# Performance work log

Measured on AMD Instinct MI355X. Metric: run time of the kernel, lower is better.

The kernel has to match this reference:

```python
import jax, jax.numpy as jnp
import numpy as np

N_NODES = 10000
N_EDGES = 160000
N_FEATS = 9       # OGB atom features
VOCAB = 128       # >= max atom feature cardinality (119)
D = 128           # d_input == d_atom_emb
H = 4             # n_heads
C = 128           # out_channels per head (== d_input)
L = 3             # n_layers
N_CLASSES = 10
NEG_SLOPE = 0.2   # PyG GATConv default


def setup_inputs() -> dict:
    key = jax.random.key(0)
    ks = jax.random.split(key, 10)
    nodes_features = jax.random.randint(ks[0], (N_NODES, N_FEATS), 0, 119, dtype=jnp.int64)
    edges_connectivity = jax.random.randint(ks[1], (2, N_EDGES), 0, N_NODES, dtype=jnp.int64)
    s = 1.0 / np.sqrt(D)
    emb_tables = jax.random.normal(ks[2], (N_FEATS, VOCAB, D), dtype=jnp.float32) * s
    W = jax.random.normal(ks[3], (L, D, H * C), dtype=jnp.float32) * s
    att_src = jax.random.normal(ks[4], (L, H, C), dtype=jnp.float32) * s
    att_dst = jax.random.normal(ks[5], (L, H, C), dtype=jnp.float32) * s
    bias = jnp.zeros((L, C), dtype=jnp.float32)
    Wc = jax.random.normal(ks[6], (D, N_CLASSES), dtype=jnp.float32) * s
    bc = jnp.zeros((N_CLASSES,), dtype=jnp.float32)
    return {"nodes_features": nodes_features, "edges_connectivity": edges_connectivity,
            "emb_tables": emb_tables, "W": W, "att_src": att_src, "att_dst": att_dst,
            "bias": bias, "Wc": Wc, "bc": bc}


def _gat_layer(x, src, dst, W_l, a_s, a_d, b_l):
    # x: [N, D] -> h: [N, H, C]
    h = (x @ W_l).reshape(-1, H, C)
    alpha_src = jnp.einsum('nhc,hc->nh', h, a_s)  # [N, H]
    alpha_dst = jnp.einsum('nhc,hc->nh', h, a_d)  # [N, H]
    e = alpha_src[src] + alpha_dst[dst]           # [E, H]
    e = jnp.where(e >= 0, e, NEG_SLOPE * e)       # LeakyReLU(0.2)
    # segment softmax over edges grouped by destination node
    m = jax.ops.segment_max(e, dst, num_segments=N_NODES)  # [N, H]
    ex = jnp.exp(e - m[dst])
    s = jax.ops.segment_sum(ex, dst, num_segments=N_NODES)  # [N, H]
    alpha = ex / (s[dst] + 1e-16)                 # [E, H]
    msg = h[src] * alpha[..., None]               # [E, H, C]
    out = jax.ops.segment_sum(msg, dst, num_segments=N_NODES)  # [N, H, C]
    return out.mean(axis=1) + b_l                 # concat=False: mean over heads


def reference(nodes_features, edges_connectivity, emb_tables, W, att_src, att_dst, bias, Wc, bc):
    # AtomEncoder: sum per-feature embeddings -> [N, D]
    x = emb_tables[jnp.arange(N_FEATS), nodes_features].sum(axis=1)
    src, dst = edges_connectivity[0], edges_connectivity[1]
    for i in range(L):
        # dropout treated as identity (eval-mode reference)
        x = _gat_layer(x, src, dst, W[i], att_src[i], att_dst[i], bias[i])
        if i < L - 1:
            x = jax.nn.gelu(x)
    pooled = x.mean(axis=0)                       # graph mean-pool over nodes -> [D]
    return pooled @ Wc + bc                       # [n_classes]
```

## Files before the change

### kernel.cpp

```cpp
#include <hip/hip_runtime.h>
#include <hip/hip_bf16.h>
#include <math.h>

#define NN 10000
#define NE 160000
#define NF 9
#define VOCAB 128
#define D 128
#define NH 4
#define C 128
#define HC 512
#define NCLS 10
#define NL 3

#define NEG_BIG (-1e30f)

typedef __attribute__((ext_vector_type(8))) short bf16x8;
typedef __attribute__((ext_vector_type(4))) float f32x4;

__device__ __forceinline__ unsigned short f2bf(float f) {
    unsigned u = __float_as_uint(f);
    unsigned r = ((u >> 16) & 1u) + 0x7FFFu;
    return (unsigned short)((u + r) >> 16);
}
__device__ __forceinline__ float bf2f(unsigned short h) {
    return __uint_as_float(((unsigned)h) << 16);
}

__global__ __launch_bounds__(256)
void hist(const int* __restrict__ dst, int* __restrict__ deg) {
    int e = blockIdx.x * 256 + threadIdx.x;
    if (e < NE) atomicAdd(&deg[dst[e]], 1);
}

#define SCAN_T 1024
#define SCAN_PER ((NN + SCAN_T - 1) / SCAN_T)
__global__ __launch_bounds__(SCAN_T)
void scan_deg(const int* __restrict__ deg, int* __restrict__ rowstart,
              int* __restrict__ cursor) {
    __shared__ int part[SCAN_T];
    int t = threadIdx.x;
    int base = t * SCAN_PER;
    int vals[SCAN_PER];
    int loc = 0;
#pragma unroll
    for (int i = 0; i < SCAN_PER; ++i) {
        int idx = base + i;
        int v = (idx < NN) ? deg[idx] : 0;
        vals[i] = v;
        loc += v;
    }
    part[t] = loc;
    __syncthreads();
    for (int off = 1; off < SCAN_T; off <<= 1) {
        int y = (t >= off) ? part[t - off] : 0;
        __syncthreads();
        part[t] += y;
        __syncthreads();
    }
    int run = part[t] - loc;
#pragma unroll
    for (int i = 0; i < SCAN_PER; ++i) {
        int idx = base + i;
        if (idx < NN) { rowstart[idx] = run; cursor[idx] = run; }
        run += vals[i];
    }
}

__global__ __launch_bounds__(256)
void scatter(const int* __restrict__ src, const int* __restrict__ dst,
             int* __restrict__ cursor, int* __restrict__ csr_src) {
    int e = blockIdx.x * 256 + threadIdx.x;
    if (e < NE) {
        int p = atomicAdd(&cursor[dst[e]], 1);
        csr_src[p] = src[e];
    }
}

__global__ __launch_bounds__(512)
void prep_all(const float* __restrict__ W, const float* __restrict__ as_,
              const float* __restrict__ ad_, const float* __restrict__ Wc,
              const float* __restrict__ biasA, const float* __restrict__ bc,
              float* __restrict__ wsrc, float* __restrict__ wdst,
              unsigned short* __restrict__ Bth, unsigned short* __restrict__ Btl,
              float* __restrict__ M, float* __restrict__ b10,
              float* __restrict__ p512) {
    int b = blockIdx.x;
    if (b < 24) {
        int k = threadIdx.x;
        if (k >= 128) return;
        int l = b >> 3;
        int r = b & 7;
        int h = r >> 1;
        int side = r & 1;
        const float* av = (side ? ad_ : as_) + (size_t)(l * NH + h) * C;
        const float* wrow = W + (size_t)l * D * HC + (size_t)k * HC + h * C;
        float acc = 0.f;
#pragma unroll 4
        for (int c = 0; c < C; ++c) acc += wrow[c] * av[c];
        float* o = (side ? wdst : wsrc) + (size_t)(l * NH + h) * D + k;
        *o = acc;
    } else if (b < 280) {
        int bb = b - 24;
        int l = bb >> 7;
        int c = bb & 127;
        int j = threadIdx.x;
        float v = W[(size_t)l * D * HC + (size_t)(j >> 2) * HC + (j & 3) * C + c];
        unsigned short h = f2bf(v);
        unsigned short lo = f2bf(v - bf2f(h));
        size_t o = (size_t)(l * 128 + c) * HC + j;
        Bth[o] = h;
        Btl[o] = lo;
    } else {
        int k = b - 280;
        int j = threadIdx.x;
        const float* W3 = W + (size_t)2 * D * HC;
        const float* bias3 = biasA + (size_t)2 * D;
        const float* wrow = W3 + (size_t)(j >> 2) * HC + (j & 3) * C;
        float acc = 0.f;
#pragma unroll 4
        for (int c = 0; c < C; ++c) acc += wrow[c] * Wc[c * NCLS + k];
        M[(size_t)k * HC + j] = acc;
        if (k == 0) p512[j] = 0.f;
        if (j == 0) {
            float bsum = bc[k];
            for (int c = 0; c < C; ++c) bsum += bias3[c] * Wc[c * NCLS + k];
            b10[k] = bsum;
        }
    }
}

__global__ __launch_bounds__(128)
void atom_encoder_alpha(const int* __restrict__ feats, const float* __restrict__ emb,
                        const float* __restrict__ wsrc0, const float* __restrict__ wdst0,
                        float* __restrict__ x, float* __restrict__ asrc,
                        float* __restrict__ adst) {
    int n = blockIdx.x;
    int t = threadIdx.x;
    __shared__ int f[NF];
    __shared__ float part[2][8];
    if (t < NF) f[t] = feats[n * NF + t];
    __syncthreads();
    float acc = 0.f;
#pragma unroll
    for (int i = 0; i < NF; ++i)
        acc += emb[(i * VOCAB + f[i]) * D + t];
    x[n * D + t] = acc;

    float dots[8];
#pragma unroll
    for (int h = 0; h < NH; ++h) {
        dots[h]     = acc * wsrc0[h * D + t];
        dots[4 + h] = acc * wdst0[h * D + t];
    }
#pragma unroll
    for (int off = 32; off; off >>= 1)
#pragma unroll
        for (int k = 0; k < 8; ++k) dots[k] += __shfl_down(dots[k], off);
    if ((t & 63) == 0) {
        int w = t >> 6;
#pragma unroll
        for (int k = 0; k < 8; ++k) part[w][k] = dots[k];
    }
    __syncthreads();
    if (t < 8) {
        float v = part[0][t] + part[1][t];
        if (t < 4) asrc[n * NH + t] = v;
        else       adst[n * NH + (t - 4)] = v;
    }
}

__global__ __launch_bounds__(256)
void alphas2(const float* __restrict__ X, const float* __restrict__ wsrc,
             const float* __restrict__ wdst, float* __restrict__ asrc,
             float* __restrict__ adst) {
    int n = blockIdx.x * 4 + (threadIdx.x >> 6);
    int lane = threadIdx.x & 63;
    float x0 = X[n * D + lane], x1 = X[n * D + lane + 64];
#pragma unroll
    for (int h = 0; h < NH; ++h) {
        float s = x0 * wsrc[h * D + lane] + x1 * wsrc[h * D + lane + 64];
        float d = x0 * wdst[h * D + lane] + x1 * wdst[h * D + lane + 64];
#pragma unroll
        for (int off = 32; off; off >>= 1) {
            s += __shfl_down(s, off);
            d += __shfl_down(d, off);
        }
        if (lane == 0) { asrc[n * NH + h] = s; adst[n * NH + h] = d; }
    }
}

__global__ __launch_bounds__(128)
void gat_agg(const int* __restrict__ csr_src, const int* __restrict__ rowstart,
             const int* __restrict__ degA, const float* __restrict__ asr,
             const float* __restrict__ adr, const float* __restrict__ X,
             unsigned* __restrict__ aggh, unsigned* __restrict__ aggl) {
    int n = blockIdx.x;
    int t = threadIdx.x;
    int deg = degA[n];
    int start = rowstart[n];

    __shared__ float smax[NH];
    __shared__ float sinv[NH];
    __shared__ float lal[128][NH];
    __shared__ int lsrc[128];

    int h = t >> 5, i = t & 31;
    float ad_h = adr[n * NH + h];
    float mx = NEG_BIG;
    for (int j = i; j < deg; j += 32) {
        int s = csr_src[start + j];
        float v = asr[s * NH + h] + ad_h;
        v = v >= 0.f ? v : 0.2f * v;
        mx = fmaxf(mx, v);
    }
#pragma unroll
    for (int off = 16; off; off >>= 1) mx = fmaxf(mx, __shfl_xor(mx, off));
    if (i == 0) smax[h] = mx;
    __syncthreads();
    float m = smax[h];
    float ss = 0.f;
    for (int j = i; j < deg; j += 32) {
        int s = csr_src[start + j];
        float v = asr[s * NH + h] + ad_h;
        v = v >= 0.f ? v : 0.2f * v;
        ss += __expf(v - m);
    }
#pragma unroll
    for (int off = 16; off; off >>= 1) ss += __shfl_xor(ss, off);
    if (i == 0) sinv[h] = 0.25f / (ss + 1e-16f);
    __syncthreads();

    float fm0 = smax[0], fm1 = smax[1], fm2 = smax[2], fm3 = smax[3];
    float fi0 = sinv[0], fi1 = sinv[1], fi2 = sinv[2], fi3 = sinv[3];
    float a0 = adr[n * NH + 0], a1 = adr[n * NH + 1];
    float a2 = adr[n * NH + 2], a3 = adr[n * NH + 3];
    float acc0 = 0.f, acc1 = 0.f, acc2 = 0.f, acc3 = 0.f;

    for (int cb = 0; cb < deg; cb += 128) {
        int cl = deg - cb; if (cl > 128) cl = 128;
        if (t < cl) {
            int sn = csr_src[start + cb + t];
            float4 av = *(const float4*)(asr + sn * NH);
            float v0 = av.x + a0; v0 = v0 >= 0.f ? v0 : 0.2f * v0;
            float v1 = av.y + a1; v1 = v1 >= 0.f ? v1 : 0.2f * v1;
            float v2 = av.z + a2; v2 = v2 >= 0.f ? v2 : 0.2f * v2;
            float v3 = av.w + a3; v3 = v3 >= 0.f ? v3 : 0.2f * v3;
            lal[t][0] = __expf(v0 - fm0) * fi0;
            lal[t][1] = __expf(v1 - fm1) * fi1;
            lal[t][2] = __expf(v2 - fm2) * fi2;
            lal[t][3] = __expf(v3 - fm3) * fi3;
            lsrc[t] = sn;
        }
        __syncthreads();
#pragma unroll 4
        for (int j = 0; j < cl; ++j) {
            float xv = X[(size_t)lsrc[j] * D + t];
            float4 w = *(const float4*)lal[j];
            acc0 += w.x * xv;
            acc1 += w.y * xv;
            acc2 += w.z * xv;
            acc3 += w.w * xv;
        }
        __syncthreads();
    }

    unsigned short h0 = f2bf(acc0), h1 = f2bf(acc1), h2 = f2bf(acc2), h3 = f2bf(acc3);
    unsigned short l0 = f2bf(acc0 - bf2f(h0)), l1 = f2bf(acc1 - bf2f(h1));
    unsigned short l2 = f2bf(acc2 - bf2f(h2)), l3 = f2bf(acc3 - bf2f(h3));
    size_t base = ((size_t)n * HC + t * 4) >> 1;
    uint2 uh = make_uint2((unsigned)h0 | ((unsigned)h1 << 16),
                          (unsigned)h2 | ((unsigned)h3 << 16));
    uint2 ul = make_uint2((unsigned)l0 | ((unsigned)l1 << 16),
                          (unsigned)l2 | ((unsigned)l3 << 16));
    *(uint2*)(aggh + base) = uh;
    *(uint2*)(aggl + base) = ul;
}

__global__ __launch_bounds__(64)
void gemm_mfma(const unsigned short* __restrict__ Ah, const unsigned short* __restrict__ Al,
               const unsigned short* __restrict__ Bth, const unsigned short* __restrict__ Btl,
               const float* __restrict__ bias, float* __restrict__ Out, int do_gelu) {
    int lane = threadIdx.x;
    int m0 = blockIdx.x * 16;
    int n0 = blockIdx.y * 64;
    int r = lane & 15;
    int g = lane >> 4;

    const bf16x8* ah = (const bf16x8*)(Ah + (size_t)(m0 + r) * HC + g * 8);
    const bf16x8* al = (const bf16x8*)(Al + (size_t)(m0 + r) * HC + g * 8);
    const bf16x8* bh0 = (const bf16x8*)(Bth + (size_t)(n0 + 0 * 16 + r) * HC + g * 8);
    const bf16x8* bh1 = (const bf16x8*)(Bth + (size_t)(n0 + 1 * 16 + r) * HC + g * 8);
    const bf16x8* bh2 = (const bf16x8*)(Bth + (size_t)(n0 + 2 * 16 + r) * HC + g * 8);
    const bf16x8* bh3 = (const bf16x8*)(Bth + (size_t)(n0 + 3 * 16 + r) * HC + g * 8);
    const bf16x8* bl0 = (const bf16x8*)(Btl + (size_t)(n0 + 0 * 16 + r) * HC + g * 8);
    const bf16x8* bl1 = (const bf16x8*)(Btl + (size_t)(n0 + 1 * 16 + r) * HC + g * 8);
    const bf16x8* bl2 = (const bf16x8*)(Btl + (size_t)(n0 + 2 * 16 + r) * HC + g * 8);
    const bf16x8* bl3 = (const bf16x8*)(Btl + (size_t)(n0 + 3 * 16 + r) * HC + g * 8);

    f32x4 acc[4];
#pragma unroll
    for (int q = 0; q < 4; ++q) acc[q] = (f32x4){0.f, 0.f, 0.f, 0.f};

#pragma unroll 2
    for (int ks = 0; ks < HC / 32; ++ks) {
        bf16x8 a_h = ah[ks * 4];
        bf16x8 a_l = al[ks * 4];
        bf16x8 b;
        b = bh0[ks * 4];
        acc[0] = __builtin_amdgcn_mfma_f32_16x16x32_bf16(a_h, b, acc[0], 0, 0, 0);
        acc[0] = __builtin_amdgcn_mfma_f32_16x16x32_bf16(a_l, b, acc[0], 0, 0, 0);
        b = bl0[ks * 4];
        acc[0] = __builtin_amdgcn_mfma_f32_16x16x32_bf16(a_h, b, acc[0], 0, 0, 0);
        b = bh1[ks * 4];
        acc[1] = __builtin_amdgcn_mfma_f32_16x16x32_bf16(a_h, b, acc[1], 0, 0, 0);
        acc[1] = __builtin_amdgcn_mfma_f32_16x16x32_bf16(a_l, b, acc[1], 0, 0, 0);
        b = bl1[ks * 4];
        acc[1] = __builtin_amdgcn_mfma_f32_16x16x32_bf16(a_h, b, acc[1], 0, 0, 0);
        b = bh2[ks * 4];
        acc[2] = __builtin_amdgcn_mfma_f32_16x16x32_bf16(a_h, b, acc[2], 0, 0, 0);
        acc[2] = __builtin_amdgcn_mfma_f32_16x16x32_bf16(a_l, b, acc[2], 0, 0, 0);
        b = bl2[ks * 4];
        acc[2] = __builtin_amdgcn_mfma_f32_16x16x32_bf16(a_h, b, acc[2], 0, 0, 0);
        b = bh3[ks * 4];
        acc[3] = __builtin_amdgcn_mfma_f32_16x16x32_bf16(a_h, b, acc[3], 0, 0, 0);
        acc[3] = __builtin_amdgcn_mfma_f32_16x16x32_bf16(a_l, b, acc[3], 0, 0, 0);
        b = bl3[ks * 4];
        acc[3] = __builtin_amdgcn_mfma_f32_16x16x32_bf16(a_h, b, acc[3], 0, 0, 0);
    }

#pragma unroll
    for (int q = 0; q < 4; ++q) {
#pragma unroll
        for (int i = 0; i < 4; ++i) {
            int row = m0 + g * 4 + i;
            int col = n0 + q * 16 + r;
            float v = acc[q][i] + bias[col];
            if (do_gelu) {
                float u = 0.7978845608028654f * (v + 0.044715f * v * v * v);
                v = 0.5f * v * (1.f + tanhf(u));
            }
            Out[(size_t)row * D + col] = v;
        }
    }
}

__global__ __launch_bounds__(512)
void pool512(const unsigned short* __restrict__ Ah, const unsigned short* __restrict__ Al,
             float* __restrict__ p) {
    int t = threadIdx.x;
    int chunk = (NN + gridDim.x - 1) / gridDim.x;
    int n0 = blockIdx.x * chunk;
    int n1 = n0 + chunk; if (n1 > NN) n1 = NN;
    float acc = 0.f;
    for (int n = n0; n < n1; ++n)
        acc += bf2f(Ah[(size_t)n * HC + t]) + bf2f(Al[(size_t)n * HC + t]);
    atomicAdd(p + t, acc);
}

__global__ __launch_bounds__(640)
void final10(const float* __restrict__ p512, const float* __restrict__ M,
             const float* __restrict__ b10, float* __restrict__ out) {
    int k = threadIdx.x >> 6;
    int lane = threadIdx.x & 63;
    float acc = 0.f;
#pragma unroll
    for (int i = 0; i < HC / 64; ++i) {
        int j = lane + i * 64;
        acc += p512[j] * M[(size_t)k * HC + j];
    }
#pragma unroll
    for (int off = 32; off; off >>= 1) acc += __shfl_down(acc, off);
    if (lane == 0) out[k] = b10[k] + acc * (1.0f / NN);
}

extern "C" void kernel_launch(void* const* d_in, const int* in_sizes, int n_in,
                              void* d_out, int out_size, void* d_ws, size_t ws_size,
                              hipStream_t stream) {
    const int*   feats = (const int*)d_in[0];
    const int*   edges = (const int*)d_in[1];
    const float* emb   = (const float*)d_in[2];
    const float* W     = (const float*)d_in[3];
    const float* asrcW = (const float*)d_in[4];
    const float* adstW = (const float*)d_in[5];
    const float* bias  = (const float*)d_in[6];
    const float* Wc    = (const float*)d_in[7];
    const float* bc    = (const float*)d_in[8];
    float* out = (float*)d_out;

    const int* srcp = edges;
    const int* dstp = edges + NE;

    char* ws = (char*)d_ws;
    size_t off = 0;
    unsigned short* aggh = (unsigned short*)(ws + off); off += (size_t)NN * HC * 2;
    unsigned short* aggl = (unsigned short*)(ws + off); off += (size_t)NN * HC * 2;
    float* xb0    = (float*)(ws + off); off += (size_t)NN * D * 4;
    float* xb1    = (float*)(ws + off); off += (size_t)NN * D * 4;
    float* asrc   = (float*)(ws + off); off += (size_t)NN * NH * 4;
    float* adst   = (float*)(ws + off); off += (size_t)NN * NH * 4;
    int*   deg    = (int*)(ws + off);   off += (size_t)NN * 4;
    int*   rowst  = (int*)(ws + off);   off += (size_t)NN * 4;
    int*   cursor = (int*)(ws + off);   off += (size_t)NN * 4;
    int*   csrsrc = (int*)(ws + off);   off += (size_t)NE * 4;
    float* wsrcb  = (float*)(ws + off); off += (size_t)NL * NH * D * 4;
    float* wdstb  = (float*)(ws + off); off += (size_t)NL * NH * D * 4;
    unsigned short* Bth = (unsigned short*)(ws + off); off += (size_t)2 * 128 * HC * 2;
    unsigned short* Btl = (unsigned short*)(ws + off); off += (size_t)2 * 128 * HC * 2;
    float* Mhead  = (float*)(ws + off); off += (size_t)NCLS * HC * 4;
    float* b10    = (float*)(ws + off); off += NCLS * 4;
    float* p512   = (float*)(ws + off); off += HC * 4;

    hipMemsetAsync(deg, 0, (size_t)NN * 4, stream);
    hist<<<(NE + 255) / 256, 256, 0, stream>>>(dstp, deg);
    scan_deg<<<1, SCAN_T, 0, stream>>>(deg, rowst, cursor);
    scatter<<<(NE + 255) / 256, 256, 0, stream>>>(srcp, dstp, cursor, csrsrc);
    prep_all<<<290, 512, 0, stream>>>(W, asrcW, adstW, Wc, bias, bc,
                                      wsrcb, wdstb, Bth, Btl, Mhead, b10, p512);

    atom_encoder_alpha<<<NN, 128, 0, stream>>>(feats, emb, wsrcb, wdstb,
                                               xb0, asrc, adst);

    float* xin = xb0;
    float* xout = xb1;
    for (int l = 0; l < 2; ++l) {
        if (l > 0)
            alphas2<<<NN / 4, 256, 0, stream>>>(xin, wsrcb + (size_t)l * NH * D,
                                                wdstb + (size_t)l * NH * D, asrc, adst);
        gat_agg<<<NN, 128, 0, stream>>>(csrsrc, rowst, deg, asrc, adst, xin,
                                        (unsigned*)aggh, (unsigned*)aggl);
        gemm_mfma<<<dim3(NN / 16, 2), 64, 0, stream>>>(
            aggh, aggl, Bth + (size_t)l * 128 * HC, Btl + (size_t)l * 128 * HC,
            bias + (size_t)l * D, xout, 1);
        float* tmp = xin; xin = xout; xout = tmp;
    }

    alphas2<<<NN / 4, 256, 0, stream>>>(xin, wsrcb + (size_t)2 * NH * D,
                                        wdstb + (size_t)2 * NH * D, asrc, adst);
    gat_agg<<<NN, 128, 0, stream>>>(csrsrc, rowst, deg, asrc, adst, xin,
                                    (unsigned*)aggh, (unsigned*)aggl);
    pool512<<<100, 512, 0, stream>>>(aggh, aggl, p512);
    final10<<<1, 640, 0, stream>>>(p512, Mhead, b10, out);
}
```

Before: 296.7 us.

## Fuse whole GAT pipeline into one cooperative persistent kernel with grid syncs

Replaces the sequence of about fifteen kernel launches (histogram, scan, scatter, prep, encoder, per-layer alphas/aggregation/GEMM, pooling, head) with a single cooperative kernel of 512 blocks that separates phases with grid-wide syncs. Aggregation now handles two nodes per 256-thread block in a grid-stride loop, and the GEMM maps four 64-thread tiles per block. The goal is to remove launch overhead and inter-kernel gaps, at the cost of grid-sync latency, lower occupancy per phase, and the added barriers in aggregation when two nodes with different degrees share a block. The old multi-kernel path is kept as a fallback if the cooperative launch fails.

After: 1.159 ms. +290.5%, slower.

```diff
diff --git a/kernel.cpp b/kernel.cpp
--- a/kernel.cpp
+++ b/kernel.cpp
@@ -1,6 +1,9 @@
 #include <hip/hip_runtime.h>
 #include <hip/hip_bf16.h>
+#include <hip/hip_cooperative_groups.h>
 #include <math.h>
+
+namespace cg = cooperative_groups;
 
 #define NN 10000
 #define NE 160000
@@ -14,6 +17,8 @@
 #define NL 3
 
 #define NEG_BIG (-1e30f)
+#define MB 512
+#define NCHUNK 20
 
 typedef __attribute__((ext_vector_type(8))) short bf16x8;
 typedef __attribute__((ext_vector_type(4))) float f32x4;
@@ -27,263 +32,125 @@
     return __uint_as_float(((unsigned)h) << 16);
 }
 
-__global__ __launch_bounds__(256)
-void hist(const int* __restrict__ dst, int* __restrict__ deg) {
-    int e = blockIdx.x * 256 + threadIdx.x;
-    if (e < NE) atomicAdd(&deg[dst[e]], 1);
-}
-
-#define SCAN_T 1024
-#define SCAN_PER ((NN + SCAN_T - 1) / SCAN_T)
-__global__ __launch_bounds__(SCAN_T)
-void scan_deg(const int* __restrict__ deg, int* __restrict__ rowstart,
-              int* __restrict__ cursor) {
-    __shared__ int part[SCAN_T];
-    int t = threadIdx.x;
-    int base = t * SCAN_PER;
-    int vals[SCAN_PER];
-    int loc = 0;
-#pragma unroll
-    for (int i = 0; i < SCAN_PER; ++i) {
-        int idx = base + i;
-        int v = (idx < NN) ? deg[idx] : 0;
-        vals[i] = v;
-        loc += v;
-    }
-    part[t] = loc;
-    __syncthreads();
-    for (int off = 1; off < SCAN_T; off <<= 1) {
-        int y = (t >= off) ? part[t - off] : 0;
+
+struct MegaParams {
+    const int* feats; const int* srcp; const int* dstp;
+    const float* emb; const float* W; const float* asrcW; const float* adstW;
+    const float* bias; const float* Wc; const float* bc;
+    float* out;
+    unsigned short *aggh, *aggl;
+    float *xb0, *xb1, *asrc, *adst;
+    int *deg, *rowst, *cursor, *csrsrc, *blocksum, *blockoff;
+    float *wsrcb, *wdstb;
+    unsigned short *Bth, *Btl;
+    float *Mhead, *b10, *p512;
+};
+
+__device__ __forceinline__ void run_agg(
+    const int* __restrict__ csr, const int* __restrict__ rowstA,
+    const int* __restrict__ degA, const float* __restrict__ asr,
+    const float* __restrict__ adr, const float* __restrict__ X,
+    unsigned* __restrict__ aggh, unsigned* __restrict__ aggl,
+    int tid, int bid,
+    float* smax, float* sinv, float* lal, int* lsrc, int* sdeg) {
+    int sub = tid >> 7, tt = tid & 127;
+    for (int base = 0; base < NN; base += MB * 2) {
+        int n = base + bid * 2 + sub;
+        bool valid = n < NN;
+        int deg = valid ? degA[n] : 0;
+        int start = valid ? rowstA[n] : 0;
+        int h = tt >> 5, i = tt & 31;
+        float ad_h = valid ? adr[n * NH + h] : 0.f;
+        float mx = NEG_BIG;
+        for (int j = i; j < deg; j += 32) {
+            int s = csr[start + j];
+            float v = asr[s * NH + h] + ad_h;
+            v = v >= 0.f ? v : 0.2f * v;
+            mx = fmaxf(mx, v);
+        }
+#pragma unroll
+        for (int off = 16; off; off >>= 1) mx = fmaxf(mx, __shfl_xor(mx, off));
+        if (i == 0) smax[sub * NH + h] = mx;
         __syncthreads();
-        part[t] += y;
+        float m = smax[sub * NH + h];
+        float ss = 0.f;
+        for (int j = i; j < deg; j += 32) {
+            int s = csr[start + j];
+            float v = asr[s * NH + h] + ad_h;
+            v = v >= 0.f ? v : 0.2f * v;
+            ss += __expf(v - m);
+        }
+#pragma unroll
+        for (int off = 16; off; off >>= 1) ss += __shfl_xor(ss, off);
+        if (i == 0) sinv[sub * NH + h] = 0.25f / (ss + 1e-16f);
+        if (tt == 0) sdeg[sub] = deg;
         __syncthreads();
-    }
-    int run = part[t] - loc;
-#pragma unroll
-    for (int i = 0; i < SCAN_PER; ++i) {
-        int idx = base + i;
-        if (idx < NN) { rowstart[idx] = run; cursor[idx] = run; }
-        run += vals[i];
-    }
-}
-
-__global__ __launch_bounds__(256)
-void scatter(const int* __restrict__ src, const int* __restrict__ dst,
-             int* __restrict__ cursor, int* __restrict__ csr_src) {
-    int e = blockIdx.x * 256 + threadIdx.x;
-    if (e < NE) {
-        int p = atomicAdd(&cursor[dst[e]], 1);
-        csr_src[p] = src[e];
-    }
-}
-
-__global__ __launch_bounds__(512)
-void prep_all(const float* __restrict__ W, const float* __restrict__ as_,
-              const float* __restrict__ ad_, const float* __restrict__ Wc,
-              const float* __restrict__ biasA, const float* __restrict__ bc,
-              float* __restrict__ wsrc, float* __restrict__ wdst,
-              unsigned short* __restrict__ Bth, unsigned short* __restrict__ Btl,
-              float* __restrict__ M, float* __restrict__ b10,
-              float* __restrict__ p512) {
-    int b = blockIdx.x;
-    if (b < 24) {
-        int k = threadIdx.x;
-        if (k >= 128) return;
-        int l = b >> 3;
-        int r = b & 7;
-        int h = r >> 1;
-        int side = r & 1;
-        const float* av = (side ? ad_ : as_) + (size_t)(l * NH + h) * C;
-        const float* wrow = W + (size_t)l * D * HC + (size_t)k * HC + h * C;
-        float acc = 0.f;
+
+        float fm0 = smax[sub * NH + 0], fm1 = smax[sub * NH + 1];
+        float fm2 = smax[sub * NH + 2], fm3 = smax[sub * NH + 3];
+        float fi0 = sinv[sub * NH + 0], fi1 = sinv[sub * NH + 1];
+        float fi2 = sinv[sub * NH + 2], fi3 = sinv[sub * NH + 3];
+        float a0 = 0.f, a1 = 0.f, a2 = 0.f, a3 = 0.f;
+        if (valid) {
+            float4 av = *(const float4*)(adr + n * NH);
+            a0 = av.x; a1 = av.y; a2 = av.z; a3 = av.w;
+        }
+        int dmax = sdeg[0] > sdeg[1] ? sdeg[0] : sdeg[1];
+        float acc0 = 0.f, acc1 = 0.f, acc2 = 0.f, acc3 = 0.f;
+        for (int cb = 0; cb < dmax; cb += 128) {
+            int cl = deg - cb; if (cl > 128) cl = 128;
+            if (tt < cl) {
+                int sn = csr[start + cb + tt];
+                float4 av = *(const float4*)(asr + sn * NH);
+                float v0 = av.x + a0; v0 = v0 >= 0.f ? v0 : 0.2f * v0;
+                float v1 = av.y + a1; v1 = v1 >= 0.f ? v1 : 0.2f * v1;
+                float v2 = av.z + a2; v2 = v2 >= 0.f ? v2 : 0.2f * v2;
+                float v3 = av.w + a3; v3 = v3 >= 0.f ? v3 : 0.2f * v3;
+                float* lp = lal + (size_t)(sub * 128 + tt) * NH;
+                lp[0] = __expf(v0 - fm0) * fi0;
+                lp[1] = __expf(v1 - fm1) * fi1;
+                lp[2] = __expf(v2 - fm2) * fi2;
+                lp[3] = __expf(v3 - fm3) * fi3;
+                lsrc[sub * 128 + tt] = sn;
+            }
+            __syncthreads();
 #pragma unroll 4
-        for (int c = 0; c < C; ++c) acc += wrow[c] * av[c];
-        float* o = (side ? wdst : wsrc) + (size_t)(l * NH + h) * D + k;
-        *o = acc;
-    } else if (b < 280) {
-        int bb = b - 24;
-        int l = bb >> 7;
-        int c = bb & 127;
-        int j = threadIdx.x;
-        float v = W[(size_t)l * D * HC + (size_t)(j >> 2) * HC + (j & 3) * C + c];
-        unsigned short h = f2bf(v);
-        unsigned short lo = f2bf(v - bf2f(h));
-        size_t o = (size_t)(l * 128 + c) * HC + j;
-        Bth[o] = h;
-        Btl[o] = lo;
-    } else {
-        int k = b - 280;
-        int j = threadIdx.x;
-        const float* W3 = W + (size_t)2 * D * HC;
-        const float* bias3 = biasA + (size_t)2 * D;
-        const float* wrow = W3 + (size_t)(j >> 2) * HC + (j & 3) * C;
-        float acc = 0.f;
-#pragma unroll 4
-        for (int c = 0; c < C; ++c) acc += wrow[c] * Wc[c * NCLS + k];
-        M[(size_t)k * HC + j] = acc;
-        if (k == 0) p512[j] = 0.f;
-        if (j == 0) {
-            float bsum = bc[k];
-            for (int c = 0; c < C; ++c) bsum += bias3[c] * Wc[c * NCLS + k];
-            b10[k] = bsum;
-        }
-    }
-}
-
-__global__ __launch_bounds__(128)
-void atom_encoder_alpha(const int* __restrict__ feats, const float* __restrict__ emb,
-                        const float* __restrict__ wsrc0, const float* __restrict__ wdst0,
-                        float* __restrict__ x, float* __restrict__ asrc,
-                        float* __restrict__ adst) {
-    int n = blockIdx.x;
-    int t = threadIdx.x;
-    __shared__ int f[NF];
-    __shared__ float part[2][8];
-    if (t < NF) f[t] = feats[n * NF + t];
-    __syncthreads();
-    float acc = 0.f;
-#pragma unroll
-    for (int i = 0; i < NF; ++i)
-        acc += emb[(i * VOCAB + f[i]) * D + t];
-    x[n * D + t] = acc;
-
-    float dots[8];
-#pragma unroll
-    for (int h = 0; h < NH; ++h) {
-        dots[h]     = acc * wsrc0[h * D + t];
-        dots[4 + h] = acc * wdst0[h * D + t];
-    }
-#pragma unroll
-    for (int off = 32; off; off >>= 1)
-#pragma unroll
-        for (int k = 0; k < 8; ++k) dots[k] += __shfl_down(dots[k], off);
-    if ((t & 63) == 0) {
-        int w = t >> 6;
-#pragma unroll
-        for (int k = 0; k < 8; ++k) part[w][k] = dots[k];
-    }
-    __syncthreads();
-    if (t < 8) {
-        float v = part[0][t] + part[1][t];
-        if (t < 4) asrc[n * NH + t] = v;
-        else       adst[n * NH + (t - 4)] = v;
-    }
-}
-
-__global__ __launch_bounds__(256)
-void alphas2(const float* __restrict__ X, const float* __restrict__ wsrc,
-             const float* __restrict__ wdst, float* __restrict__ asrc,
-             float* __restrict__ adst) {
-    int n = blockIdx.x * 4 + (threadIdx.x >> 6);
-    int lane = threadIdx.x & 63;
-    float x0 = X[n * D + lane], x1 = X[n * D + lane + 64];
-#pragma unroll
-    for (int h = 0; h < NH; ++h) {
-        float s = x0 * wsrc[h * D + lane] + x1 * wsrc[h * D + lane + 64];
-        float d = x0 * wdst[h * D + lane] + x1 * wdst[h * D + lane + 64];
-#pragma unroll
-        for (int off = 32; off; off >>= 1) {
-            s += __shfl_down(s, off);
-            d += __shfl_down(d, off);
-        }
-        if (lane == 0) { asrc[n * NH + h] = s; adst[n * NH + h] = d; }
-    }
-}
-
-__global__ __launch_bounds__(128)
-void gat_agg(const int* __restrict__ csr_src, const int* __restrict__ rowstart,
-             const int* __restrict__ degA, const float* __restrict__ asr,
-             const float* __restrict__ adr, const float* __restrict__ X,
-             unsigned* __restrict__ aggh, unsigned* __restrict__ aggl) {
-    int n = blockIdx.x;
-    int t = threadIdx.x;
-    int deg = degA[n];
-    int start = rowstart[n];
-
-    __shared__ float smax[NH];
-    __shared__ float sinv[NH];
-    __shared__ float lal[128][NH];
-    __shared__ int lsrc[128];
-
-    int h = t >> 5, i = t & 31;
-    float ad_h = adr[n * NH + h];
-    float mx = NEG_BIG;
-    for (int j = i; j < deg; j += 32) {
-        int s = csr_src[start + j];
-        float v = asr[s * NH + h] + ad_h;
-        v = v >= 0.f ? v : 0.2f * v;
-        mx = fmaxf(mx, v);
-    }
-#pragma unroll
-    for (int off = 16; off; off >>= 1) mx = fmaxf(mx, __shfl_xor(mx, off));
-    if (i == 0) smax[h] = mx;
-    __syncthreads();
-    float m = smax[h];
-    float ss = 0.f;
-    for (int j = i; j < deg; j += 32) {
-        int s = csr_src[start + j];
-        float v = asr[s * NH + h] + ad_h;
-        v = v >= 0.f ? v : 0.2f * v;
-        ss += __expf(v - m);
-    }
-#pragma unroll
-    for (int off = 16; off; off >>= 1) ss += __shfl_xor(ss, off);
-    if (i == 0) sinv[h] = 0.25f / (ss + 1e-16f);
-    __syncthreads();
-
-    float fm0 = smax[0], fm1 = smax[1], fm2 = smax[2], fm3 = smax[3];
-    float fi0 = sinv[0], fi1 = sinv[1], fi2 = sinv[2], fi3 = sinv[3];
-    float a0 = adr[n * NH + 0], a1 = adr[n * NH + 1];
-    float a2 = adr[n * NH + 2], a3 = adr[n * NH + 3];
-    float acc0 = 0.f, acc1 = 0.f, acc2 = 0.f, acc3 = 0.f;
-
-    for (int cb = 0; cb < deg; cb += 128) {
-        int cl = deg - cb; if (cl > 128) cl = 128;
-        if (t < cl) {
-            int sn = csr_src[start + cb + t];
-            float4 av = *(const float4*)(asr + sn * NH);
-            float v0 = av.x + a0; v0 = v0 >= 0.f ? v0 : 0.2f * v0;
-            float v1 = av.y + a1; v1 = v1 >= 0.f ? v1 : 0.2f * v1;
-            float v2 = av.z + a2; v2 = v2 >= 0.f ? v2 : 0.2f * v2;
-            float v3 = av.w + a3; v3 = v3 >= 0.f ? v3 : 0.2f * v3;
-            lal[t][0] = __expf(v0 - fm0) * fi0;
-            lal[t][1] = __expf(v1 - fm1) * fi1;
-            lal[t][2] = __expf(v2 - fm2) * fi2;
-            lal[t][3] = __expf(v3 - fm3) * fi3;
-            lsrc[t] = sn;
+            for (int j = 0; j < cl; ++j) {
+                float xv = X[(size_t)lsrc[sub * 128 + j] * D + tt];
+                float4 w = *(const float4*)(lal + (size_t)(sub * 128 + j) * NH);
+                acc0 += w.x * xv;
+                acc1 += w.y * xv;
+                acc2 += w.z * xv;
+                acc3 += w.w * xv;
+            }
+            __syncthreads();
+        }
+        if (valid) {
+            unsigned short h0 = f2bf(acc0), h1 = f2bf(acc1), h2 = f2bf(acc2), h3 = f2bf(acc3);
+            unsigned short l0 = f2bf(acc0 - bf2f(h0)), l1 = f2bf(acc1 - bf2f(h1));
+            unsigned short l2 = f2bf(acc2 - bf2f(h2)), l3 = f2bf(acc3 - bf2f(h3));
+            size_t bofs = ((size_t)n * HC + tt * 4) >> 1;
+            uint2 uh = make_uint2((unsigned)h0 | ((unsigned)h1 << 16),
+                                  (unsigned)h2 | ((unsigned)h3 << 16));
+            uint2 ul = make_uint2((unsigned)l0 | ((unsigned)l1 << 16),
+                                  (unsigned)l2 | ((unsigned)l3 << 16));
+            *(uint2*)((unsigned*)aggh + bofs) = uh;
+            *(uint2*)((unsigned*)aggl + bofs) = ul;
         }
         __syncthreads();
-#pragma unroll 4
-        for (int j = 0; j < cl; ++j) {
-            float xv = X[(size_t)lsrc[j] * D + t];
-            float4 w = *(const float4*)lal[j];
-            acc0 += w.x * xv;
-            acc1 += w.y * xv;
-            acc2 += w.z * xv;
-            acc3 += w.w * xv;
-        }
-        __syncthreads();
-    }
-
-    unsigned short h0 = f2bf(acc0), h1 = f2bf(acc1), h2 = f2bf(acc2), h3 = f2bf(acc3);
-    unsigned short l0 = f2bf(acc0 - bf2f(h0)), l1 = f2bf(acc1 - bf2f(h1));
-    unsigned short l2 = f2bf(acc2 - bf2f(h2)), l3 = f2bf(acc3 - bf2f(h3));
-    size_t base = ((size_t)n * HC + t * 4) >> 1;
-    uint2 uh = make_uint2((unsigned)h0 | ((unsigned)h1 << 16),
-                          (unsigned)h2 | ((unsigned)h3 << 16));
-    uint2 ul = make_uint2((unsigned)l0 | ((unsigned)l1 << 16),
-                          (unsigned)l2 | ((unsigned)l3 << 16));
-    *(uint2*)(aggh + base) = uh;
-    *(uint2*)(aggl + base) = ul;
-}
-
-__global__ __launch_bounds__(64)
-void gemm_mfma(const unsigned short* __restrict__ Ah, const unsigned short* __restrict__ Al,
-               const unsigned short* __restrict__ Bth, const unsigned short* __restrict__ Btl,
-               const float* __restrict__ bias, float* __restrict__ Out, int do_gelu) {
-    int lane = threadIdx.x;
-    int m0 = blockIdx.x * 16;
-    int n0 = blockIdx.y * 64;
+    }
+}
+
+__device__ __forceinline__ void run_gemm(
+    const unsigned short* __restrict__ Ah, const unsigned short* __restrict__ Al,
+    const unsigned short* __restrict__ Bth, const unsigned short* __restrict__ Btl,
+    const float* __restrict__ bias, float* __restrict__ Out,
+    int tid, int bid) {
+    int tile = bid * 4 + (tid >> 6);
+    if (tile >= (NN / 16) * 2) return;
+    int lane = tid & 63;
+    int m0 = (tile >> 1) * 16;
+    int n0 = (tile & 1) * 64;
     int r = lane & 15;
     int g = lane >> 4;
 
@@ -336,6 +203,537 @@
             int row = m0 + g * 4 + i;
             int col = n0 + q * 16 + r;
             float v = acc[q][i] + bias[col];
+            float u = 0.7978845608028654f * (v + 0.044715f * v * v * v);
+            v = 0.5f * v * (1.f + tanhf(u));
+            Out[(size_t)row * D + col] = v;
+        }
+    }
+}
+
+__device__ __forceinline__ void run_alphas(
+    const float* __restrict__ X, const float* __restrict__ wsrc,
+    const float* __restrict__ wdst, float* __restrict__ asrc,
+    float* __restrict__ adst, int tid, int bid) {
+    int lane = tid & 63;
+    for (int base = 0; base < NN; base += MB * 4) {
+        int n = base + bid * 4 + (tid >> 6);
+        if (n >= NN) continue;
+        float x0 = X[n * D + lane], x1 = X[n * D + lane + 64];
+#pragma unroll
+        for (int h = 0; h < NH; ++h) {
+            float s = x0 * wsrc[h * D + lane] + x1 * wsrc[h * D + lane + 64];
+            float d = x0 * wdst[h * D + lane] + x1 * wdst[h * D + lane + 64];
+#pragma unroll
+            for (int off = 32; off; off >>= 1) {
+                s += __shfl_down(s, off);
+                d += __shfl_down(d, off);
+            }
+            if (lane == 0) { asrc[n * NH + h] = s; adst[n * NH + h] = d; }
+        }
+    }
+}
+
+__global__ __launch_bounds__(256, 2)
+void mega(MegaParams p) {
+    cg::grid_group grid = cg::this_grid();
+    const int tid = threadIdx.x;
+    const int bid = blockIdx.x;
+    const int gtid = bid * 256 + tid;
+    const int gsz = MB * 256;
+
+    __shared__ int s_scan[256];
+    __shared__ int s_f[2][NF];
+    __shared__ float s_part[2][2][8];
+    __shared__ float s_smax[2 * NH];
+    __shared__ float s_sinv[2 * NH];
+    __shared__ float s_lal[2 * 128 * NH];
+    __shared__ int s_lsrc[2 * 128];
+    __shared__ int s_sdeg[2];
+
+    for (int i = gtid; i < NN; i += gsz) p.deg[i] = 0;
+    grid.sync();
+
+    for (int e = gtid; e < NE; e += gsz) atomicAdd(&p.deg[p.dstp[e]], 1);
+    grid.sync();
+
+    {
+        int n0 = bid * NCHUNK;
+        int v = 0;
+        if (tid < NCHUNK && n0 + tid < NN) v = p.deg[n0 + tid];
+        if (tid < 64) {
+#pragma unroll
+            for (int off = 32; off; off >>= 1) v += __shfl_down(v, off);
+            if (tid == 0) p.blocksum[bid] = v;
+        }
+    }
+    grid.sync();
+
+    if (bid == 0) {
+        int a = p.blocksum[2 * tid], b2 = p.blocksum[2 * tid + 1];
+        int pr = a + b2;
+        s_scan[tid] = pr;
+        __syncthreads();
+        for (int off = 1; off < 256; off <<= 1) {
+            int val = (tid >= off) ? s_scan[tid - off] : 0;
+            __syncthreads();
+            s_scan[tid] += val;
+            __syncthreads();
+        }
+        int ep = s_scan[tid] - pr;
+        p.blockoff[2 * tid] = ep;
+        p.blockoff[2 * tid + 1] = ep + a;
+    }
+    grid.sync();
+
+    if (tid == 0) {
+        int run = p.blockoff[bid];
+        int n0 = bid * NCHUNK;
+        for (int i = 0; i < NCHUNK; ++i) {
+            int idx = n0 + i;
+            if (idx < NN) { p.rowst[idx] = run; p.cursor[idx] = run; run += p.deg[idx]; }
+        }
+    }
+    for (int u = bid; u < 24 + 512 + 20; u += MB) {
+        if (u < 24) {
+            if (tid < 128) {
+                int k = tid;
+                int l = u >> 3, r = u & 7, h = r >> 1, side = r & 1;
+                const float* av = (side ? p.adstW : p.asrcW) + (size_t)(l * NH + h) * C;
+                const float* wrow = p.W + (size_t)l * D * HC + (size_t)k * HC + h * C;
+                float acc = 0.f;
+#pragma unroll 4
+                for (int c = 0; c < C; ++c) acc += wrow[c] * av[c];
+                float* o = (side ? p.wdstb : p.wsrcb) + (size_t)(l * NH + h) * D + k;
+                *o = acc;
+            }
+        } else if (u < 536) {
+            int w = u - 24;
+            int l = w >> 8, c = (w & 255) >> 1, jh = w & 1;
+            int j = jh * 256 + tid;
+            float v = p.W[(size_t)l * D * HC + (size_t)(j >> 2) * HC + (j & 3) * C + c];
+            unsigned short h = f2bf(v);
+            unsigned short lo = f2bf(v - bf2f(h));
+            size_t o = (size_t)(l * 128 + c) * HC + j;
+            p.Bth[o] = h;
+            p.Btl[o] = lo;
+        } else {
+            int hu = u - 536;
+            int k = hu >> 1, jh = hu & 1;
+            int j = jh * 256 + tid;
+            const float* W3 = p.W + (size_t)2 * D * HC;
+            const float* wrow = W3 + (size_t)(j >> 2) * HC + (j & 3) * C;
+            float acc = 0.f;
+#pragma unroll 4
+            for (int c = 0; c < C; ++c) acc += wrow[c] * p.Wc[c * NCLS + k];
+            p.Mhead[(size_t)k * HC + j] = acc;
+            if (k == 0) p.p512[j] = 0.f;
+            if (j == 0) {
+                const float* bias3 = p.bias + (size_t)2 * D;
+                float bsum = p.bc[k];
+                for (int c = 0; c < C; ++c) bsum += bias3[c] * p.Wc[c * NCLS + k];
+                p.b10[k] = bsum;
+            }
+        }
+    }
+    grid.sync();
+
+    for (int e = gtid; e < NE; e += gsz) {
+        int pos = atomicAdd(&p.cursor[p.dstp[e]], 1);
+        p.csrsrc[pos] = p.srcp[e];
+    }
+    {
+        int sub = tid >> 7, tt = tid & 127;
+        for (int base = 0; base < NN; base += MB * 2) {
+            int n = base + bid * 2 + sub;
+            bool valid = n < NN;
+            if (valid && tt < NF) s_f[sub][tt] = p.feats[n * NF + tt];
+            __syncthreads();
+            float dots[8];
+#pragma unroll
+            for (int k = 0; k < 8; ++k) dots[k] = 0.f;
+            if (valid) {
+                float acc = 0.f;
+#pragma unroll
+                for (int i = 0; i < NF; ++i)
+                    acc += p.emb[(i * VOCAB + s_f[sub][i]) * D + tt];
+                p.xb0[n * D + tt] = acc;
+#pragma unroll
+                for (int h = 0; h < NH; ++h) {
+                    dots[h]     = acc * p.wsrcb[h * D + tt];
+                    dots[4 + h] = acc * p.wdstb[h * D + tt];
+                }
+            }
+#pragma unroll
+            for (int off = 32; off; off >>= 1)
+#pragma unroll
+                for (int k = 0; k < 8; ++k) dots[k] += __shfl_down(dots[k], off);
+            if ((tt & 63) == 0) {
+#pragma unroll
+                for (int k = 0; k < 8; ++k) s_part[sub][tt >> 6][k] = dots[k];
+            }
+            __syncthreads();
+            if (valid && tt < 8) {
+                float v = s_part[sub][0][tt] + s_part[sub][1][tt];
+                if (tt < 4) p.asrc[n * NH + tt] = v;
+                else        p.adst[n * NH + (tt - 4)] = v;
+            }
+            __syncthreads();
+        }
+    }
+    grid.sync();
+
+    run_agg(p.csrsrc, p.rowst, p.deg, p.asrc, p.adst, p.xb0,
+            (unsigned*)p.aggh, (unsigned*)p.aggl, tid, bid,
+            s_smax, s_sinv, s_lal, s_lsrc, s_sdeg);
+    grid.sync();
+    run_gemm(p.aggh, p.aggl, p.Bth, p.Btl, p.bias, p.xb1, tid, bid);
+    grid.sync();
+    run_alphas(p.xb1, p.wsrcb + (size_t)1 * NH * D, p.wdstb + (size_t)1 * NH * D,
+               p.asrc, p.adst, tid, bid);
+    grid.sync();
+
+    run_agg(p.csrsrc, p.rowst, p.deg, p.asrc, p.adst, p.xb1,
+            (unsigned*)p.aggh, (unsigned*)p.aggl, tid, bid,
+            s_smax, s_sinv, s_lal, s_lsrc, s_sdeg);
+    grid.sync();
+    run_gemm(p.aggh, p.aggl, p.Bth + (size_t)128 * HC, p.Btl + (size_t)128 * HC,
+             p.bias + (size_t)1 * D, p.xb0, tid, bid);
+    grid.sync();
+    run_alphas(p.xb0, p.wsrcb + (size_t)2 * NH * D, p.wdstb + (size_t)2 * NH * D,
+               p.asrc, p.adst, tid, bid);
+    grid.sync();
+
+    run_agg(p.csrsrc, p.rowst, p.deg, p.asrc, p.adst, p.xb0,
+            (unsigned*)p.aggh, (unsigned*)p.aggl, tid, bid,
+            s_smax, s_sinv, s_lal, s_lsrc, s_sdeg);
+    grid.sync();
+    {
+        int n0 = bid * NCHUNK;
+        float a0 = 0.f, a1 = 0.f;
+        for (int i = 0; i < NCHUNK; ++i) {
+            int idx = n0 + i;
+            if (idx < NN) {
+                a0 += bf2f(p.aggh[(size_t)idx * HC + tid]) + bf2f(p.aggl[(size_t)idx * HC + tid]);
+                a1 += bf2f(p.aggh[(size_t)idx * HC + tid + 256]) + bf2f(p.aggl[(size_t)idx * HC + tid + 256]);
+            }
+        }
+        atomicAdd(p.p512 + tid, a0);
+        atomicAdd(p.p512 + tid + 256, a1);
+    }
+    grid.sync();
+
+    if (bid == 0) {
+        int k = tid >> 4, i = tid & 15;
+        if (k < NCLS) {
+            float acc = 0.f;
+#pragma unroll 8
+            for (int q = 0; q < HC / 16; ++q) {
+                int j = i + q * 16;
+                acc += p.p512[j] * p.Mhead[(size_t)k * HC + j];
+            }
+#pragma unroll
+            for (int off = 8; off; off >>= 1) acc += __shfl_down(acc, off, 16);
+            if (i == 0) p.out[k] = p.b10[k] + acc * (1.0f / NN);
+        }
+    }
+}
+
+
+__global__ __launch_bounds__(256)
+void hist(const int* __restrict__ dst, int* __restrict__ deg) {
+    int e = blockIdx.x * 256 + threadIdx.x;
+    if (e < NE) atomicAdd(&deg[dst[e]], 1);
+}
+
+#define SCAN_T 1024
+#define SCAN_PER ((NN + SCAN_T - 1) / SCAN_T)
+__global__ __launch_bounds__(SCAN_T)
+void scan_deg(const int* __restrict__ deg, int* __restrict__ rowstart,
+              int* __restrict__ cursor) {
+    __shared__ int part[SCAN_T];
+    int t = threadIdx.x;
+    int base = t * SCAN_PER;
+    int vals[SCAN_PER];
+    int loc = 0;
+#pragma unroll
+    for (int i = 0; i < SCAN_PER; ++i) {
+        int idx = base + i;
+        int v = (idx < NN) ? deg[idx] : 0;
+        vals[i] = v;
+        loc += v;
+    }
+    part[t] = loc;
+    __syncthreads();
+    for (int off = 1; off < SCAN_T; off <<= 1) {
+        int y = (t >= off) ? part[t - off] : 0;
+        __syncthreads();
+        part[t] += y;
+        __syncthreads();
+    }
+    int run = part[t] - loc;
+#pragma unroll
+    for (int i = 0; i < SCAN_PER; ++i) {
+        int idx = base + i;
+        if (idx < NN) { rowstart[idx] = run; cursor[idx] = run; }
+        run += vals[i];
+    }
+}
+
+__global__ __launch_bounds__(256)
+void scatter(const int* __restrict__ src, const int* __restrict__ dst,
+             int* __restrict__ cursor, int* __restrict__ csr_src) {
+    int e = blockIdx.x * 256 + threadIdx.x;
+    if (e < NE) {
+        int p = atomicAdd(&cursor[dst[e]], 1);
+        csr_src[p] = src[e];
+    }
+}
+
+__global__ __launch_bounds__(512)
+void prep_all(const float* __restrict__ W, const float* __restrict__ as_,
+              const float* __restrict__ ad_, const float* __restrict__ Wc,
+              const float* __restrict__ biasA, const float* __restrict__ bc,
+              float* __restrict__ wsrc, float* __restrict__ wdst,
+              unsigned short* __restrict__ Bth, unsigned short* __restrict__ Btl,
+              float* __restrict__ M, float* __restrict__ b10,
+              float* __restrict__ p512) {
+    int b = blockIdx.x;
+    if (b < 24) {
+        int k = threadIdx.x;
+        if (k >= 128) return;
+        int l = b >> 3, r = b & 7, h = r >> 1, side = r & 1;
+        const float* av = (side ? ad_ : as_) + (size_t)(l * NH + h) * C;
+        const float* wrow = W + (size_t)l * D * HC + (size_t)k * HC + h * C;
+        float acc = 0.f;
+#pragma unroll 4
+        for (int c = 0; c < C; ++c) acc += wrow[c] * av[c];
+        float* o = (side ? wdst : wsrc) + (size_t)(l * NH + h) * D + k;
+        *o = acc;
+    } else if (b < 280) {
+        int bb = b - 24;
+        int l = bb >> 7, c = bb & 127;
+        int j = threadIdx.x;
+        float v = W[(size_t)l * D * HC + (size_t)(j >> 2) * HC + (j & 3) * C + c];
+        unsigned short h = f2bf(v);
+        unsigned short lo = f2bf(v - bf2f(h));
+        size_t o = (size_t)(l * 128 + c) * HC + j;
+        Bth[o] = h;
+        Btl[o] = lo;
+    } else {
+        int k = b - 280;
+        int j = threadIdx.x;
+        const float* W3 = W + (size_t)2 * D * HC;
+        const float* bias3 = biasA + (size_t)2 * D;
+        const float* wrow = W3 + (size_t)(j >> 2) * HC + (j & 3) * C;
+        float acc = 0.f;
+#pragma unroll 4
+        for (int c = 0; c < C; ++c) acc += wrow[c] * Wc[c * NCLS + k];
+        M[(size_t)k * HC + j] = acc;
+        if (k == 0) p512[j] = 0.f;
+        if (j == 0) {
+            float bsum = bc[k];
+            for (int c = 0; c < C; ++c) bsum += bias3[c] * Wc[c * NCLS + k];
+            b10[k] = bsum;
+        }
+    }
+}
+
+__global__ __launch_bounds__(128)
+void atom_encoder_alpha(const int* __restrict__ feats, const float* __restrict__ emb,
+                        const float* __restrict__ wsrc0, const float* __restrict__ wdst0,
+                        float* __restrict__ x, float* __restrict__ asrc,
+                        float* __restrict__ adst) {
+    int n = blockIdx.x;
+    int t = threadIdx.x;
+    __shared__ int f[NF];
+    __shared__ float part[2][8];
+    if (t < NF) f[t] = feats[n * NF + t];
+    __syncthreads();
+    float acc = 0.f;
+#pragma unroll
+    for (int i = 0; i < NF; ++i)
+        acc += emb[(i * VOCAB + f[i]) * D + t];
+    x[n * D + t] = acc;
+    float dots[8];
+#pragma unroll
+    for (int h = 0; h < NH; ++h) {
+        dots[h]     = acc * wsrc0[h * D + t];
+        dots[4 + h] = acc * wdst0[h * D + t];
+    }
+#pragma unroll
+    for (int off = 32; off; off >>= 1)
+#pragma unroll
+        for (int k = 0; k < 8; ++k) dots[k] += __shfl_down(dots[k], off);
+    if ((t & 63) == 0) {
+        int w = t >> 6;
+#pragma unroll
+        for (int k = 0; k < 8; ++k) part[w][k] = dots[k];
+    }
+    __syncthreads();
+    if (t < 8) {
+        float v = part[0][t] + part[1][t];
+        if (t < 4) asrc[n * NH + t] = v;
+        else       adst[n * NH + (t - 4)] = v;
+    }
+}
+
+__global__ __launch_bounds__(256)
+void alphas2(const float* __restrict__ X, const float* __restrict__ wsrc,
+             const float* __restrict__ wdst, float* __restrict__ asrc,
+             float* __restrict__ adst) {
+    int n = blockIdx.x * 4 + (threadIdx.x >> 6);
+    int lane = threadIdx.x & 63;
+    float x0 = X[n * D + lane], x1 = X[n * D + lane + 64];
+#pragma unroll
+    for (int h = 0; h < NH; ++h) {
+        float s = x0 * wsrc[h * D + lane] + x1 * wsrc[h * D + lane + 64];
+        float d = x0 * wdst[h * D + lane] + x1 * wdst[h * D + lane + 64];
+#pragma unroll
+        for (int off = 32; off; off >>= 1) {
+            s += __shfl_down(s, off);
+            d += __shfl_down(d, off);
+        }
+        if (lane == 0) { asrc[n * NH + h] = s; adst[n * NH + h] = d; }
+    }
+}
+
+__global__ __launch_bounds__(128)
+void gat_agg(const int* __restrict__ csr_src, const int* __restrict__ rowstart,
+             const int* __restrict__ degA, const float* __restrict__ asr,
+             const float* __restrict__ adr, const float* __restrict__ X,
+             unsigned* __restrict__ aggh, unsigned* __restrict__ aggl) {
+    int n = blockIdx.x;
+    int t = threadIdx.x;
+    int deg = degA[n];
+    int start = rowstart[n];
+    __shared__ float smax[NH];
+    __shared__ float sinv[NH];
+    __shared__ float lal[128][NH];
+    __shared__ int lsrc[128];
+    int h = t >> 5, i = t & 31;
+    float ad_h = adr[n * NH + h];
+    float mx = NEG_BIG;
+    for (int j = i; j < deg; j += 32) {
+        int s = csr_src[start + j];
+        float v = asr[s * NH + h] + ad_h;
+        v = v >= 0.f ? v : 0.2f * v;
+        mx = fmaxf(mx, v);
+    }
+#pragma unroll
+    for (int off = 16; off; off >>= 1) mx = fmaxf(mx, __shfl_xor(mx, off));
+    if (i == 0) smax[h] = mx;
+    __syncthreads();
+    float m = smax[h];
+    float ss = 0.f;
+    for (int j = i; j < deg; j += 32) {
+        int s = csr_src[start + j];
+        float v = asr[s * NH + h] + ad_h;
+        v = v >= 0.f ? v : 0.2f * v;
+        ss += __expf(v - m);
+    }
+#pragma unroll
+    for (int off = 16; off; off >>= 1) ss += __shfl_xor(ss, off);
+    if (i == 0) sinv[h] = 0.25f / (ss + 1e-16f);
+    __syncthreads();
+    float fm0 = smax[0], fm1 = smax[1], fm2 = smax[2], fm3 = smax[3];
+    float fi0 = sinv[0], fi1 = sinv[1], fi2 = sinv[2], fi3 = sinv[3];
+    float a0 = adr[n * NH + 0], a1 = adr[n * NH + 1];
+    float a2 = adr[n * NH + 2], a3 = adr[n * NH + 3];
+    float acc0 = 0.f, acc1 = 0.f, acc2 = 0.f, acc3 = 0.f;
+    for (int cb = 0; cb < deg; cb += 128) {
+        int cl = deg - cb; if (cl > 128) cl = 128;
+        if (t < cl) {
+            int sn = csr_src[start + cb + t];
+            float4 av = *(const float4*)(asr + sn * NH);
+            float v0 = av.x + a0; v0 = v0 >= 0.f ? v0 : 0.2f * v0;
+            float v1 = av.y + a1; v1 = v1 >= 0.f ? v1 : 0.2f * v1;
+            float v2 = av.z + a2; v2 = v2 >= 0.f ? v2 : 0.2f * v2;
+            float v3 = av.w + a3; v3 = v3 >= 0.f ? v3 : 0.2f * v3;
+            lal[t][0] = __expf(v0 - fm0) * fi0;
+            lal[t][1] = __expf(v1 - fm1) * fi1;
+            lal[t][2] = __expf(v2 - fm2) * fi2;
+            lal[t][3] = __expf(v3 - fm3) * fi3;
+            lsrc[t] = sn;
+        }
+        __syncthreads();
+#pragma unroll 4
+        for (int j = 0; j < cl; ++j) {
+            float xv = X[(size_t)lsrc[j] * D + t];
+            float4 w = *(const float4*)lal[j];
+            acc0 += w.x * xv;
+            acc1 += w.y * xv;
+            acc2 += w.z * xv;
+            acc3 += w.w * xv;
+        }
+        __syncthreads();
+    }
+    unsigned short h0 = f2bf(acc0), h1 = f2bf(acc1), h2 = f2bf(acc2), h3 = f2bf(acc3);
+    unsigned short l0 = f2bf(acc0 - bf2f(h0)), l1 = f2bf(acc1 - bf2f(h1));
+    unsigned short l2 = f2bf(acc2 - bf2f(h2)), l3 = f2bf(acc3 - bf2f(h3));
+    size_t base = ((size_t)n * HC + t * 4) >> 1;
+    uint2 uh = make_uint2((unsigned)h0 | ((unsigned)h1 << 16),
+                          (unsigned)h2 | ((unsigned)h3 << 16));
+    uint2 ul = make_uint2((unsigned)l0 | ((unsigned)l1 << 16),
+                          (unsigned)l2 | ((unsigned)l3 << 16));
+    *(uint2*)(aggh + base) = uh;
+    *(uint2*)(aggl + base) = ul;
+}
+
+__global__ __launch_bounds__(64)
+void gemm_mfma(const unsigned short* __restrict__ Ah, const unsigned short* __restrict__ Al,
+               const unsigned short* __restrict__ Bth, const unsigned short* __restrict__ Btl,
+               const float* __restrict__ bias, float* __restrict__ Out, int do_gelu) {
+    int lane = threadIdx.x;
+    int m0 = blockIdx.x * 16;
+    int n0 = blockIdx.y * 64;
+    int r = lane & 15;
+    int g = lane >> 4;
+    const bf16x8* ah = (const bf16x8*)(Ah + (size_t)(m0 + r) * HC + g * 8);
+    const bf16x8* al = (const bf16x8*)(Al + (size_t)(m0 + r) * HC + g * 8);
+    const bf16x8* bh0 = (const bf16x8*)(Bth + (size_t)(n0 + 0 * 16 + r) * HC + g * 8);
+    const bf16x8* bh1 = (const bf16x8*)(Bth + (size_t)(n0 + 1 * 16 + r) * HC + g * 8);
+    const bf16x8* bh2 = (const bf16x8*)(Bth + (size_t)(n0 + 2 * 16 + r) * HC + g * 8);
+    const bf16x8* bh3 = (const bf16x8*)(Bth + (size_t)(n0 + 3 * 16 + r) * HC + g * 8);
+    const bf16x8* bl0 = (const bf16x8*)(Btl + (size_t)(n0 + 0 * 16 + r) * HC + g * 8);
+    const bf16x8* bl1 = (const bf16x8*)(Btl + (size_t)(n0 + 1 * 16 + r) * HC + g * 8);
+    const bf16x8* bl2 = (const bf16x8*)(Btl + (size_t)(n0 + 2 * 16 + r) * HC + g * 8);
+    const bf16x8* bl3 = (const bf16x8*)(Btl + (size_t)(n0 + 3 * 16 + r) * HC + g * 8);
+    f32x4 acc[4];
+#pragma unroll
+    for (int q = 0; q < 4; ++q) acc[q] = (f32x4){0.f, 0.f, 0.f, 0.f};
+#pragma unroll 2
+    for (int ks = 0; ks < HC / 32; ++ks) {
+        bf16x8 a_h = ah[ks * 4];
+        bf16x8 a_l = al[ks * 4];
+        bf16x8 b;
+        b = bh0[ks * 4];
+        acc[0] = __builtin_amdgcn_mfma_f32_16x16x32_bf16(a_h, b, acc[0], 0, 0, 0);
+        acc[0] = __builtin_amdgcn_mfma_f32_16x16x32_bf16(a_l, b, acc[0], 0, 0, 0);
+        b = bl0[ks * 4];
+        acc[0] = __builtin_amdgcn_mfma_f32_16x16x32_bf16(a_h, b, acc[0], 0, 0, 0);
+        b = bh1[ks * 4];
+        acc[1] = __builtin_amdgcn_mfma_f32_16x16x32_bf16(a_h, b, acc[1], 0, 0, 0);
+        acc[1] = __builtin_amdgcn_mfma_f32_16x16x32_bf16(a_l, b, acc[1], 0, 0, 0);
+        b = bl1[ks * 4];
+        acc[1] = __builtin_amdgcn_mfma_f32_16x16x32_bf16(a_h, b, acc[1], 0, 0, 0);
+        b = bh2[ks * 4];
+        acc[2] = __builtin_amdgcn_mfma_f32_16x16x32_bf16(a_h, b, acc[2], 0, 0, 0);
+        acc[2] = __builtin_amdgcn_mfma_f32_16x16x32_bf16(a_l, b, acc[2], 0, 0, 0);
+        b = bl2[ks * 4];
+        acc[2] = __builtin_amdgcn_mfma_f32_16x16x32_bf16(a_h, b, acc[2], 0, 0, 0);
+        b = bh3[ks * 4];
+        acc[3] = __builtin_amdgcn_mfma_f32_16x16x32_bf16(a_h, b, acc[3], 0, 0, 0);
+        acc[3] = __builtin_amdgcn_mfma_f32_16x16x32_bf16(a_l, b, acc[3], 0, 0, 0);
+        b = bl3[ks * 4];
+        acc[3] = __builtin_amdgcn_mfma_f32_16x16x32_bf16(a_h, b, acc[3], 0, 0, 0);
+    }
+#pragma unroll
+    for (int q = 0; q < 4; ++q) {
+#pragma unroll
+        for (int i = 0; i < 4; ++i) {
+            int row = m0 + g * 4 + i;
+            int col = n0 + q * 16 + r;
+            float v = acc[q][i] + bias[col];
             if (do_gelu) {
                 float u = 0.7978845608028654f * (v + 0.044715f * v * v * v);
                 v = 0.5f * v * (1.f + tanhf(u));
@@ -408,8 +806,25 @@
     unsigned short* Bth = (unsigned short*)(ws + off); off += (size_t)2 * 128 * HC * 2;
     unsigned short* Btl = (unsigned short*)(ws + off); off += (size_t)2 * 128 * HC * 2;
     float* Mhead  = (float*)(ws + off); off += (size_t)NCLS * HC * 4;
-    float* b10    = (float*)(ws + off); off += NCLS * 4;
+    float* b10    = (float*)(ws + off); off += (size_t)((NCLS + 127) / 128) * 128 * 4;
     float* p512   = (float*)(ws + off); off += HC * 4;
+    int*   blocksum = (int*)(ws + off); off += (size_t)MB * 4;
+    int*   blockoff = (int*)(ws + off); off += (size_t)MB * 4;
+
+    MegaParams mp;
+    mp.feats = feats; mp.srcp = srcp; mp.dstp = dstp;
+    mp.emb = emb; mp.W = W; mp.asrcW = asrcW; mp.adstW = adstW;
+    mp.bias = bias; mp.Wc = Wc; mp.bc = bc; mp.out = out;
+    mp.aggh = aggh; mp.aggl = aggl; mp.xb0 = xb0; mp.xb1 = xb1;
+    mp.asrc = asrc; mp.adst = adst; mp.deg = deg; mp.rowst = rowst;
+    mp.cursor = cursor; mp.csrsrc = csrsrc; mp.blocksum = blocksum;
+    mp.blockoff = blockoff; mp.wsrcb = wsrcb; mp.wdstb = wdstb;
+    mp.Bth = Bth; mp.Btl = Btl; mp.Mhead = Mhead; mp.b10 = b10; mp.p512 = p512;
+
+    void* args[] = {(void*)&mp};
+    hipError_t err = hipLaunchCooperativeKernel((const void*)mega, dim3(MB), dim3(256),
+                                                args, 0, stream);
+    if (err == hipSuccess) return;
 
     hipMemsetAsync(deg, 0, (size_t)NN * 4, stream);
     hist<<<(NE + 255) / 256, 256, 0, stream>>>(dstp, deg);
@@ -417,10 +832,8 @@
     scatter<<<(NE + 255) / 256, 256, 0, stream>>>(srcp, dstp, cursor, csrsrc);
     prep_all<<<290, 512, 0, stream>>>(W, asrcW, adstW, Wc, bias, bc,
                                       wsrcb, wdstb, Bth, Btl, Mhead, b10, p512);
-
     atom_encoder_alpha<<<NN, 128, 0, stream>>>(feats, emb, wsrcb, wdstb,
                                                xb0, asrc, adst);
-
     float* xin = xb0;
     float* xout = xb1;
     for (int l = 0; l < 2; ++l) {
@@ -434,7 +847,6 @@
             bias + (size_t)l * D, xout, 1);
         float* tmp = xin; xin = xout; xout = tmp;
     }
-
     alphas2<<<NN / 4, 256, 0, stream>>>(xin, wsrcb + (size_t)2 * NH * D,
                                         wdstb + (size_t)2 * NH * D, asrc, adst);
     gat_agg<<<NN, 128, 0, stream>>>(csrsrc, rowst, deg, asrc, adst, xin,
```
